# Kernel tuning notes

Hardware: AMD Instinct MI355X
Metric: run time of the kernel (lower is better)

## Reference

```python
import jax, jax.numpy as jnp
import numpy as np

M = 1024      # num_inducing
B = 131072    # batch of query points (original module is per-query; we vmap/vectorize)
EPS_D = 1e-8
JITTER = 1e-4

Z_SCALE = np.array([0.15, 0.1, 0.05, 800.0, 20.0], dtype=np.float32)
Z_SHIFT = np.array([0.0, 0.0, 0.0, 600.0, 5.0], dtype=np.float32)


def setup_inputs() -> dict:
    key = jax.random.key(0)
    k1, k2 = jax.random.split(key)
    x_star = jax.random.normal(k1, (B, 5), dtype=jnp.float32)
    # learnable params, sized/initialized per the flax module
    log_lengthscale = jnp.log(jnp.array([0.2, 0.15, 0.1, 400.0, 15.0], dtype=jnp.float32))
    log_variance = jnp.asarray(jnp.log(0.08), dtype=jnp.float32)
    Z_raw = jax.random.uniform(k2, (M, 5), dtype=jnp.float32)  # uniform(scale=1.0) init
    return {"x_star": x_star, "log_lengthscale": log_lengthscale,
            "log_variance": log_variance, "Z_raw": Z_raw}


def _pairwise_sqdist(A, Bm):
    # ||a-b||^2 via gemm; A:(n,d), Bm:(m,d) -> (n,m)
    aa = jnp.sum(A * A, axis=-1)
    bb = jnp.sum(Bm * Bm, axis=-1)
    d2 = aa[:, None] + bb[None, :] - 2.0 * (A @ Bm.T)
    return jnp.maximum(d2, 0.0)


def _matern52(d2, prior_var):
    d = jnp.sqrt(d2 + EPS_D)
    s = jnp.sqrt(5.0) * d
    return prior_var * (1.0 + s + (5.0 / 3.0) * (d * d)) * jnp.exp(-s)


def reference(x_star, log_lengthscale, log_variance, Z_raw):
    ls = jnp.exp(log_lengthscale)                # (5,)
    prior_var = jnp.exp(log_variance)            # scalar
    Z = Z_raw * jnp.asarray(Z_SCALE) + jnp.asarray(Z_SHIFT)  # (M,5)
    inv_ls = 1.0 / (ls + 1e-8)
    Zs = Z * inv_ls                              # lengthscale-scaled inducing pts
    Xs = x_star * inv_ls                         # (B,5)

    K_ZZ = _matern52(_pairwise_sqdist(Zs, Zs), prior_var)            # (M,M)
    K_ZZ_inv = jnp.linalg.inv(K_ZZ + JITTER * jnp.eye(M, dtype=K_ZZ.dtype))

    k_xZ = _matern52(_pairwise_sqdist(Xs, Zs), prior_var)            # (B,M)
    red = jnp.sum(k_xZ * (k_xZ @ K_ZZ_inv), axis=-1)                 # (B,)
    variance = jnp.maximum(prior_var - red, 1e-6)
    return jnp.sqrt(variance)                                        # (B,) predictive std
```

## Files before the change

### kernel.cpp

```cpp
#include <hip/hip_runtime.h>
#include <math.h>

#define B_TOT 131072
#define M_N   1024
#define BS    128
#define NBK   8

typedef float    f32x4 __attribute__((ext_vector_type(4)));
typedef _Float16 f16x8 __attribute__((ext_vector_type(8)));

enum : size_t {
    OFF_KF  = 0,
    OFF_LF  = (size_t)4 << 20,
    OFF_WF  = (size_t)8 << 20,
    OFF_WPH = (size_t)12 << 20,
    OFF_WPL = (size_t)14 << 20,
    OFF_RED = (size_t)16 << 20,
    OFF_PF  = (size_t)17 << 20,
    OFF_ZT  = ((size_t)17 << 20) + 256,
};

__device__ __constant__ float c_zscale[5] = {0.15f, 0.1f, 0.05f, 800.0f, 20.0f};
__device__ __constant__ float c_zshift[5] = {0.0f, 0.0f, 0.0f, 600.0f, 5.0f};

__global__ __launch_bounds__(256) void k_build(const float* __restrict__ log_ls,
                                               const float* __restrict__ log_var,
                                               const float* __restrict__ Zraw,
                                               float* __restrict__ Kf,
                                               float* __restrict__ pf,
                                               float* __restrict__ Zst) {
    __shared__ float ps[6];
    __shared__ float zsi[5];
    int tid = threadIdx.x;
    if (tid < 5) ps[tid] = 1.0f / (__expf(log_ls[tid]) + 1e-8f);
    if (tid == 5) ps[5] = __expf(log_var[0]);
    __syncthreads();
    int i = blockIdx.x >> 2;
    int j = (blockIdx.x & 3) * 256 + tid;
    if (tid < 5) zsi[tid] = (Zraw[i * 5 + tid] * c_zscale[tid] + c_zshift[tid]) * ps[tid];
    __syncthreads();
    float d2 = 0.0f;
#pragma unroll
    for (int d = 0; d < 5; ++d) {
        float zj = (Zraw[j * 5 + d] * c_zscale[d] + c_zshift[d]) * ps[d];
        float df = zsi[d] - zj;
        d2 += df * df;
    }
    float dd = d2 + 1e-8f;
    float dist = sqrtf(dd);
    float s = 2.23606798f * dist;
    float v = ps[5] * (1.0f + s + 1.66666667f * dd) * __expf(-s);
    if (i == j) v += 1e-4f;
    Kf[(size_t)i * M_N + j] = v;
    if (blockIdx.x < 4) {
        int m = blockIdx.x * 256 + tid;
#pragma unroll
        for (int d = 0; d < 5; ++d)
            Zst[d * M_N + m] = (Zraw[m * 5 + d] * c_zscale[d] + c_zshift[d]) * ps[d];
    }
    if (blockIdx.x == 4 && tid < 6) pf[tid] = ps[tid];
}

__global__ __launch_bounds__(512) void kw_diag(float* __restrict__ Kf,
                                               float* __restrict__ Wf, int kb) {
    __shared__ float As[128][129];
    __shared__ float sinv[128];
    int tid = threadIdx.x;
    int r0 = kb * BS;
    for (int idx = tid; idx < BS * BS; idx += 512) {
        int rr = idx >> 7, cc = idx & 127;
        As[rr][cc] = Kf[(size_t)(r0 + rr) * M_N + r0 + cc];
    }
    __syncthreads();

    int r = tid & 127, q = tid >> 7;
    for (int p = 0; p < 16; ++p) {
        int j0 = p * 8;
        for (int j = j0; j < j0 + 8; ++j) {
            if (tid == j) {
                float d = sqrtf(As[j][j]);
                As[j][j] = d;
                sinv[j] = 1.0f / d;
            }
            __syncthreads();
            float arj = 0.0f;
            if (q == 0 && r > j) {
                arj = As[r][j] * sinv[j];
                As[r][j] = arj;
            }
            __syncthreads();
            if (q == 0 && r > j) {
#pragma unroll
                for (int c = j + 1; c < j0 + 8; ++c)
                    As[r][c] -= arj * As[c][j];
            }
        }
        __syncthreads();
        if (p < 15) {
            float a[8];
#pragma unroll
            for (int t = 0; t < 8; ++t) a[t] = As[r][j0 + t];
            for (int c = j0 + 8 + q; c < 128; c += 4) {
                if (r >= c) {
                    float s = As[r][c];
#pragma unroll
                    for (int t = 0; t < 8; ++t) s -= a[t] * As[c][j0 + t];
                    As[r][c] = s;
                }
            }
        }
        __syncthreads();
    }

    if (tid < 128) {
        int c = tid;
        for (int rb = 0; rb < 16; ++rb) {
            int r0b = rb * 8;
            if (c >= r0b + 8) continue;
            float s[8];
#pragma unroll
            for (int i = 0; i < 8; ++i) s[i] = 0.0f;
            for (int t = 0; t < r0b; ++t) {
                if (t >= c) {
                    float xt = (t == c) ? sinv[c] : As[c][t];
#pragma unroll
                    for (int i = 0; i < 8; ++i) s[i] += As[r0b + i][t] * xt;
                }
            }
            float xloc[8];
#pragma unroll
            for (int i = 0; i < 8; ++i) {
                int rr = r0b + i;
                float v = 0.0f;
                if (rr >= c) {
                    v = ((rr == c) ? 1.0f : 0.0f) - s[i];
#pragma unroll
                    for (int t2 = 0; t2 < i; ++t2) {
                        int tt = r0b + t2;
                        if (tt >= c) v -= As[rr][tt] * xloc[t2];
                    }
                    v *= sinv[rr];
                    if (rr > c) As[c][rr] = v;
                }
                xloc[i] = v;
            }
        }
    }
    __syncthreads();
    for (int idx = tid; idx < BS * BS; idx += 512) {
        int rr = idx >> 7, cc = idx & 127;
        if (rr >= cc)
            Wf[(size_t)(r0 + rr) * M_N + r0 + cc] = (rr == cc) ? sinv[rr] : As[cc][rr];
    }
}

static __device__ void d_strip(const float* __restrict__ Kf, const float* __restrict__ Wf,
                               int cb, int row0, float (*S)[129],
                               float (*Ast)[17], float (*Wst)[128], int tid) {
    int c = tid & 127, q = tid >> 7;
    float acc[32];
#pragma unroll
    for (int i = 0; i < 32; ++i) acc[i] = 0.0f;
    for (int tc = 0; tc < 8; ++tc) {
        int tb = tc * 16;
        __syncthreads();
        for (int idx = tid; idx < 64 * 16; idx += 256) {
            int rr = idx >> 4, tt = idx & 15;
            Ast[rr][tt] = Kf[(size_t)(row0 + rr) * M_N + cb + tb + tt];
        }
        for (int idx = tid; idx < 128 * 16; idx += 256) {
            int cc = idx >> 4, tt = idx & 15;
            Wst[tt][cc] = (tb + tt <= cc) ? Wf[(size_t)(cb + cc) * M_N + cb + tb + tt] : 0.0f;
        }
        __syncthreads();
#pragma unroll
        for (int t = 0; t < 16; ++t) {
            float w = Wst[t][c];
#pragma unroll
            for (int i = 0; i < 32; ++i) acc[i] += Ast[q * 32 + i][t] * w;
        }
    }
#pragma unroll
    for (int i = 0; i < 32; ++i) S[q * 32 + i][c] = acc[i];
}

__global__ __launch_bounds__(256) void kw_step(float* __restrict__ Kf,
                                               const float* __restrict__ Wf,
                                               float* __restrict__ Lf, int kb) {
    __shared__ float SA[64][129];
    __shared__ float SB[64][129];
    __shared__ float Ast[64][17];
    __shared__ float Wst[16][128];
    int tid = threadIdx.x;
    int v = blockIdx.x;
    int by = 0;
    while ((by + 1) * (by + 2) / 2 <= v) ++by;
    int bx = v - by * (by + 1) / 2;
    int base = (kb + 1) * BS;
    int cb = kb * BS;
    int gr0 = base + by * 64, gc0 = base + bx * 64;

    d_strip(Kf, Wf, cb, gr0, SA, Ast, Wst, tid);
    if (bx != by) d_strip(Kf, Wf, cb, gc0, SB, Ast, Wst, tid);
    float (*PB)[129] = (bx == by) ? SA : SB;
    __syncthreads();

    int tx = tid & 15, ty = tid >> 4;
    float acc[4][4];
#pragma unroll
    for (int i = 0; i < 4; ++i)
#pragma unroll
        for (int j = 0; j < 4; ++j) acc[i][j] = 0.0f;
    for (int t = 0; t < 128; ++t) {
        float a[4], b[4];
#pragma unroll
        for (int i = 0; i < 4; ++i) a[i] = SA[ty * 4 + i][t];
#pragma unroll
        for (int j = 0; j < 4; ++j) b[j] = PB[tx * 4 + j][t];
#pragma unroll
        for (int i = 0; i < 4; ++i)
#pragma unroll
            for (int j = 0; j < 4; ++j) acc[i][j] = fmaf(a[i], b[j], acc[i][j]);
    }
#pragma unroll
    for (int i = 0; i < 4; ++i)
#pragma unroll
        for (int j = 0; j < 4; ++j)
            Kf[(size_t)(gr0 + ty * 4 + i) * M_N + gc0 + tx * 4 + j] -= acc[i][j];

    if (by == bx) {
        for (int idx = tid; idx < 64 * 128; idx += 256)
            Lf[(size_t)(gr0 + (idx >> 7)) * M_N + cb + (idx & 127)] = SA[idx >> 7][idx & 127];
    }
}

__global__ __launch_bounds__(512) void kw_trtri(const float* __restrict__ Lf,
                                                float* __restrict__ Wf) {
    __shared__ float Ls[128][33];
    __shared__ float Ws[32][33];
    __shared__ float Whist[6][128][33];
    __shared__ float Ps[128][33];
    int j  = blockIdx.y;
    int ct = blockIdx.x;
    int c0 = j * BS + ct * 32;
    int tid = threadIdx.x;
    int rq = tid >> 2, cq = tid & 3;

    for (int i = j + 1; i < 8; ++i) {
        float acc[8];
#pragma unroll
        for (int c = 0; c < 8; ++c) acc[c] = 0.0f;
        for (int t = j; t < i; ++t) {
            for (int ch = 0; ch < 4; ++ch) {
                int tb = t * BS + ch * 32;
                __syncthreads();
                for (int idx = tid; idx < 128 * 32; idx += 512) {
                    int rr = idx >> 5, tt = idx & 31;
                    Ls[rr][tt] = Lf[(size_t)(i * BS + rr) * M_N + tb + tt];
                }
                if (t == j) {
                    for (int idx = tid; idx < 32 * 32; idx += 512) {
                        int tt = idx >> 5, cc = idx & 31;
                        int gr = tb + tt, gc = c0 + cc;
                        Ws[tt][cc] = (gr >= gc) ? Wf[(size_t)gr * M_N + gc] : 0.0f;
                    }
                }
                __syncthreads();
                if (t == j) {
#pragma unroll
                    for (int tt = 0; tt < 32; ++tt) {
                        float l = Ls[rq][tt];
#pragma unroll
                        for (int c = 0; c < 8; ++c)
                            acc[c] = fmaf(l, Ws[tt][cq * 8 + c], acc[c]);
                    }
                } else {
                    const float (*Wh)[33] = Whist[t - j - 1];
#pragma unroll
                    for (int tt = 0; tt < 32; ++tt) {
                        float l = Ls[rq][tt];
#pragma unroll
                        for (int c = 0; c < 8; ++c)
                            acc[c] = fmaf(l, Wh[ch * 32 + tt][cq * 8 + c], acc[c]);
                    }
                }
            }
        }
        __syncthreads();
#pragma unroll
        for (int c = 0; c < 8; ++c) Ps[rq][cq * 8 + c] = acc[c];
        float a2[8];
#pragma unroll
        for (int c = 0; c < 8; ++c) a2[c] = 0.0f;
        for (int ch = 0; ch < 4; ++ch) {
            __syncthreads();
            for (int idx = tid; idx < 128 * 32; idx += 512) {
                int rr = idx >> 5, tt = idx & 31;
                Ls[rr][tt] = (rr >= ch * 32 + tt)
                           ? Wf[(size_t)(i * BS + rr) * M_N + i * BS + ch * 32 + tt] : 0.0f;
            }
            __syncthreads();
#pragma unroll
            for (int tt = 0; tt < 32; ++tt) {
                float l = Ls[rq][tt];
#pragma unroll
                for (int c = 0; c < 8; ++c)
                    a2[c] = fmaf(l, Ps[ch * 32 + tt][cq * 8 + c], a2[c]);
            }
        }
        __syncthreads();
#pragma unroll
        for (int c = 0; c < 8; ++c) {
            float v = -a2[c];
            Wf[(size_t)(i * BS + rq) * M_N + c0 + cq * 8 + c] = v;
            if (i < 7) Whist[i - j - 1][rq][cq * 8 + c] = v;
        }
        __syncthreads();
    }
}

__global__ void kw_pack(const float* __restrict__ Wf, _Float16* __restrict__ Wph,
                        _Float16* __restrict__ Wpl) {
    int T = blockIdx.x * 256 + threadIdx.x;
    int lane = T & 63, fid = T >> 6;
    int jn = fid & 63, kik = fid >> 6;
    int ki = kik & 3, kc = kik >> 2;
    int j  = jn * 16 + (lane & 15);
    int kb = kc * 128 + ki * 32 + (lane >> 4) * 8;
    f16x8 h, lo;
#pragma unroll
    for (int e = 0; e < 8; ++e) {
        int k = kb + e;
        float v = (k <= j) ? Wf[(size_t)j * M_N + k] : 0.0f;
        _Float16 hh = (_Float16)v;
        h[e]  = hh;
        lo[e] = (_Float16)(v - (float)hh);
    }
    size_t off = (size_t)fid * 512 + lane * 8;
    *(f16x8*)(Wph + off) = h;
    *(f16x8*)(Wpl + off) = lo;
}

__global__ __launch_bounds__(256) void k_mm(const float* __restrict__ x_star,
                                            const float* __restrict__ pf,
                                            const float* __restrict__ Zst,
                                            const _Float16* __restrict__ Wph,
                                            const _Float16* __restrict__ Wpl,
                                            float* __restrict__ redp, int Bq) {
    __shared__ __align__(16) char kls[32 * 256];
    __shared__ float red_l[32];
    int tid  = threadIdx.x;
    int slab = blockIdx.x, pp = blockIdx.y;
    int w = tid >> 6, lane = tid & 63;
    int lrow = lane & 15, kgrp = lane >> 4;

    int srow = tid >> 3, sg = tid & 7;
    int qrow = slab * 32 + srow;
    int qc = (qrow < Bq) ? qrow : (Bq - 1);
    float xv0 = x_star[(size_t)qc * 5 + 0] * pf[0];
    float xv1 = x_star[(size_t)qc * 5 + 1] * pf[1];
    float xv2 = x_star[(size_t)qc * 5 + 2] * pf[2];
    float xv3 = x_star[(size_t)qc * 5 + 3] * pf[3];
    float xv4 = x_star[(size_t)qc * 5 + 4] * pf[4];
    float pv = pf[5];
    if (tid < 32) red_l[tid] = 0.0f;

    f32x4 acc[2][8];
#pragma unroll
    for (int mi = 0; mi < 2; ++mi)
#pragma unroll
        for (int nj = 0; nj < 8; ++nj) acc[mi][nj] = (f32x4)(0.0f);

    int jmax_w = (pp * 32 + 28 + ((w + 3) & 3)) * 16 + 15;
    int KC = pp ? 8 : 4;

    for (int kc = 0; kc < KC; ++kc) {
        f16x8 hv[2];
#pragma unroll
        for (int b = 0; b < 2; ++b) {
            int lb = kc * 128 + sg * 16 + b * 8;
            float z0[8], z1[8], z2[8], z3[8], z4[8];
            *(float4*)&z0[0] = *(const float4*)&Zst[lb];
            *(float4*)&z0[4] = *(const float4*)&Zst[lb + 4];
            *(float4*)&z1[0] = *(const float4*)&Zst[M_N + lb];
            *(float4*)&z1[4] = *(const float4*)&Zst[M_N + lb + 4];
            *(float4*)&z2[0] = *(const float4*)&Zst[2 * M_N + lb];
            *(float4*)&z2[4] = *(const float4*)&Zst[2 * M_N + lb + 4];
            *(float4*)&z3[0] = *(const float4*)&Zst[3 * M_N + lb];
            *(float4*)&z3[4] = *(const float4*)&Zst[3 * M_N + lb + 4];
            *(float4*)&z4[0] = *(const float4*)&Zst[4 * M_N + lb];
            *(float4*)&z4[4] = *(const float4*)&Zst[4 * M_N + lb + 4];
#pragma unroll
            for (int e = 0; e < 8; ++e) {
                float dx0 = xv0 - z0[e], dx1 = xv1 - z1[e], dx2 = xv2 - z2[e],
                      dx3 = xv3 - z3[e], dx4 = xv4 - z4[e];
                float d2 = dx0 * dx0 + dx1 * dx1 + dx2 * dx2 + dx3 * dx3 + dx4 * dx4;
                float ddv = d2 + 1e-8f;
                float dist = sqrtf(ddv);
                float sv = 2.23606798f * dist;
                hv[b][e] = (_Float16)(pv * (1.0f + sv + 1.66666667f * ddv) * __expf(-sv));
            }
        }
        __syncthreads();
        {
            int o0 = srow * 256 + ((sg * 32) ^ ((srow & 15) << 4));
            int o1 = srow * 256 + ((sg * 32 + 16) ^ ((srow & 15) << 4));
            *(f16x8*)(&kls[o0]) = hv[0];
            *(f16x8*)(&kls[o1]) = hv[1];
        }
        __syncthreads();

        for (int ki = 0; ki < 4; ++ki) {
            int kmin = kc * 128 + ki * 32;
            if (kmin > jmax_w) break;
            f16x8 A_[2];
#pragma unroll
            for (int mi = 0; mi < 2; ++mi) {
                int row = mi * 16 + lrow;
                int cb  = ki * 64 + kgrp * 16;
                A_[mi] = *(const f16x8*)(&kls[row * 256 + (cb ^ ((row & 15) << 4))]);
            }
#pragma unroll
            for (int nj = 0; nj < 8; ++nj) {
                int jng = pp * 32 + nj * 4 + ((w + nj) & 3);
                if (kmin > jng * 16 + 15) continue;
                size_t fo = ((size_t)((kc * 4 + ki) * 64 + jng)) * 512 + lane * 8;
                f16x8 Bh = *(const f16x8*)(Wph + fo);
                f16x8 Bl = *(const f16x8*)(Wpl + fo);
#pragma unroll
                for (int mi = 0; mi < 2; ++mi) {
                    acc[mi][nj] = __builtin_amdgcn_mfma_f32_16x16x32_f16(A_[mi], Bh, acc[mi][nj], 0, 0, 0);
                    acc[mi][nj] = __builtin_amdgcn_mfma_f32_16x16x32_f16(A_[mi], Bl, acc[mi][nj], 0, 0, 0);
                }
            }
        }
    }

#pragma unroll
    for (int mi = 0; mi < 2; ++mi) {
#pragma unroll
        for (int q = 0; q < 4; ++q) {
            float s = 0.0f;
#pragma unroll
            for (int nj = 0; nj < 8; ++nj) s = fmaf(acc[mi][nj][q], acc[mi][nj][q], s);
            s += __shfl_xor(s, 1);
            s += __shfl_xor(s, 2);
            s += __shfl_xor(s, 4);
            s += __shfl_xor(s, 8);
            if (lrow == 0) atomicAdd(&red_l[mi * 16 + kgrp * 4 + q], s);
        }
    }
    __syncthreads();
    if (tid < 32) {
        int b = slab * 32 + tid;
        if (b < Bq) redp[(size_t)pp * Bq + b] = red_l[tid];
    }
}

__global__ void k_fin(const float* __restrict__ redp, const float* __restrict__ pf,
                      float* __restrict__ out, int Bq) {
    int b = blockIdx.x * 256 + threadIdx.x;
    if (b < Bq) {
        float red = redp[b] + redp[(size_t)Bq + b];
        out[b] = sqrtf(fmaxf(pf[5] - red, 1e-6f));
    }
}

extern "C" void kernel_launch(void* const* d_in, const int* in_sizes, int n_in,
                              void* d_out, int out_size, void* d_ws, size_t ws_size,
                              hipStream_t stream) {
    const float* x_star  = (const float*)d_in[0];
    const float* log_ls  = (const float*)d_in[1];
    const float* log_var = (const float*)d_in[2];
    const float* Z_raw   = (const float*)d_in[3];
    float* out = (float*)d_out;
    int Bq = in_sizes[0] / 5;

    char* ws = (char*)d_ws;
    float*     Kf   = (float*)(ws + OFF_KF);
    float*     Lf   = (float*)(ws + OFF_LF);
    float*     Wf   = (float*)(ws + OFF_WF);
    _Float16*  Wph  = (_Float16*)(ws + OFF_WPH);
    _Float16*  Wpl  = (_Float16*)(ws + OFF_WPL);
    float*     redp = (float*)(ws + OFF_RED);
    float*     pf   = (float*)(ws + OFF_PF);
    float*     Zst  = (float*)(ws + OFF_ZT);

    k_build<<<4096, 256, 0, stream>>>(log_ls, log_var, Z_raw, Kf, pf, Zst);

    for (int kb = 0; kb < NBK; ++kb) {
        kw_diag<<<1, 512, 0, stream>>>(Kf, Wf, kb);
        int R = M_N - (kb + 1) * BS;
        if (R > 0) {
            int nt = R / 64;
            kw_step<<<nt * (nt + 1) / 2, 256, 0, stream>>>(Kf, Wf, Lf, kb);
        }
    }
    kw_trtri<<<dim3(4, 7), 512, 0, stream>>>(Lf, Wf);
    kw_pack<<<512, 256, 0, stream>>>(Wf, Wph, Wpl);

    int slabs = (Bq + 31) / 32;
    k_mm<<<dim3(slabs, 2), 256, 0, stream>>>(x_star, pf, Zst, Wph, Wpl, redp, Bq);
    k_fin<<<(Bq + 255) / 256, 256, 0, stream>>>(redp, pf, out, Bq);
}
```

Before: 3.555 ms.

## Fuse diagonal factor into step kernel and restructure main MFMA kernel

The blocked Cholesky loop now folds the next diagonal-block factorization and inversion into block 0 of each trailing-update launch, so the separate per-step diag launches go away. The main kernel handles 64 query rows per 512-thread block instead of splitting columns across two blocks with 32 rows each. It also double-buffers the on-the-fly k_xZ tile in LDS so tile generation overlaps the MFMAs, and writes the final sqrt directly, dropping the partial-sum buffer and finalize kernel. The cost is more registers and LDS per block (launch bounds 512,1), lower occupancy, and a serial 256-thread diagonal factorization on the critical path of each step.

Result: slower. 3.680 ms (+3.5%).

```diff
diff --git a/kernel.cpp b/kernel.cpp
--- a/kernel.cpp
+++ b/kernel.cpp
@@ -15,9 +15,8 @@
     OFF_WF  = (size_t)8 << 20,
     OFF_WPH = (size_t)12 << 20,
     OFF_WPL = (size_t)14 << 20,
-    OFF_RED = (size_t)16 << 20,
-    OFF_PF  = (size_t)17 << 20,
-    OFF_ZT  = ((size_t)17 << 20) + 256,
+    OFF_PF  = (size_t)16 << 20,
+    OFF_ZT  = ((size_t)16 << 20) + 256,
 };
 
 __device__ __constant__ float c_zscale[5] = {0.15f, 0.1f, 0.05f, 800.0f, 20.0f};
@@ -180,57 +179,184 @@
             for (int i = 0; i < 32; ++i) acc[i] += Ast[q * 32 + i][t] * w;
         }
     }
+    __syncthreads();
 #pragma unroll
     for (int i = 0; i < 32; ++i) S[q * 32 + i][c] = acc[i];
 }
 
+static __device__ void d_diag256(float (*As)[129], float* sinv,
+                                 float* __restrict__ Wf, int r0, int tid) {
+    int r = tid & 127, half = tid >> 7;
+    for (int p = 0; p < 16; ++p) {
+        int j0 = p * 8;
+        for (int j = j0; j < j0 + 8; ++j) {
+            if (tid == j) {
+                float d = sqrtf(As[j][j]);
+                As[j][j] = d;
+                sinv[j] = 1.0f / d;
+            }
+            __syncthreads();
+            float arj = 0.0f;
+            if (half == 0 && r > j) {
+                arj = As[r][j] * sinv[j];
+                As[r][j] = arj;
+            }
+            __syncthreads();
+            if (half == 0 && r > j) {
+#pragma unroll
+                for (int c = j + 1; c < j0 + 8; ++c)
+                    As[r][c] -= arj * As[c][j];
+            }
+        }
+        __syncthreads();
+        if (p < 15) {
+            float a[8];
+#pragma unroll
+            for (int t = 0; t < 8; ++t) a[t] = As[r][j0 + t];
+            for (int c = j0 + 8 + half; c < 128; c += 2) {
+                if (r >= c) {
+                    float s = As[r][c];
+#pragma unroll
+                    for (int t = 0; t < 8; ++t) s -= a[t] * As[c][j0 + t];
+                    As[r][c] = s;
+                }
+            }
+        }
+        __syncthreads();
+    }
+    if (tid < 128) {
+        int c = tid;
+        for (int rb = 0; rb < 16; ++rb) {
+            int r0b = rb * 8;
+            if (c >= r0b + 8) continue;
+            float s[8];
+#pragma unroll
+            for (int i = 0; i < 8; ++i) s[i] = 0.0f;
+            for (int t = 0; t < r0b; ++t) {
+                if (t >= c) {
+                    float xt = (t == c) ? sinv[c] : As[c][t];
+#pragma unroll
+                    for (int i = 0; i < 8; ++i) s[i] += As[r0b + i][t] * xt;
+                }
+            }
+            float xloc[8];
+#pragma unroll
+            for (int i = 0; i < 8; ++i) {
+                int rr = r0b + i;
+                float v = 0.0f;
+                if (rr >= c) {
+                    v = ((rr == c) ? 1.0f : 0.0f) - s[i];
+#pragma unroll
+                    for (int t2 = 0; t2 < i; ++t2) {
+                        int tt = r0b + t2;
+                        if (tt >= c) v -= As[rr][tt] * xloc[t2];
+                    }
+                    v *= sinv[rr];
+                    if (rr > c) As[c][rr] = v;
+                }
+                xloc[i] = v;
+            }
+        }
+    }
+    __syncthreads();
+    for (int idx = tid; idx < BS * BS; idx += 256) {
+        int rr = idx >> 7, cc = idx & 127;
+        if (rr >= cc)
+            Wf[(size_t)(r0 + rr) * M_N + r0 + cc] = (rr == cc) ? sinv[rr] : As[cc][rr];
+    }
+}
+
 __global__ __launch_bounds__(256) void kw_step(float* __restrict__ Kf,
-                                               const float* __restrict__ Wf,
+                                               float* __restrict__ Wf,
                                                float* __restrict__ Lf, int kb) {
     __shared__ float SA[64][129];
     __shared__ float SB[64][129];
     __shared__ float Ast[64][17];
     __shared__ float Wst[16][128];
+    __shared__ float As[128][129];
+    __shared__ float sinv[128];
     int tid = threadIdx.x;
-    int v = blockIdx.x;
-    int by = 0;
-    while ((by + 1) * (by + 2) / 2 <= v) ++by;
-    int bx = v - by * (by + 1) / 2;
     int base = (kb + 1) * BS;
     int cb = kb * BS;
-    int gr0 = base + by * 64, gc0 = base + bx * 64;
-
-    d_strip(Kf, Wf, cb, gr0, SA, Ast, Wst, tid);
-    if (bx != by) d_strip(Kf, Wf, cb, gc0, SB, Ast, Wst, tid);
-    float (*PB)[129] = (bx == by) ? SA : SB;
-    __syncthreads();
-
     int tx = tid & 15, ty = tid >> 4;
-    float acc[4][4];
-#pragma unroll
-    for (int i = 0; i < 4; ++i)
-#pragma unroll
-        for (int j = 0; j < 4; ++j) acc[i][j] = 0.0f;
-    for (int t = 0; t < 128; ++t) {
-        float a[4], b[4];
-#pragma unroll
-        for (int i = 0; i < 4; ++i) a[i] = SA[ty * 4 + i][t];
-#pragma unroll
-        for (int j = 0; j < 4; ++j) b[j] = PB[tx * 4 + j][t];
+
+    if (blockIdx.x == 0) {
+        d_strip(Kf, Wf, cb, base, SA, Ast, Wst, tid);
+        d_strip(Kf, Wf, cb, base + 64, SB, Ast, Wst, tid);
+        __syncthreads();
+#pragma unroll
+        for (int qq = 0; qq < 3; ++qq) {
+            int qy = (qq == 0) ? 0 : 1;
+            int qx = (qq == 2) ? 1 : 0;
+            float (*Sy)[129] = qy ? SB : SA;
+            float (*Sx)[129] = qx ? SB : SA;
+            float acc[4][4];
+#pragma unroll
+            for (int i = 0; i < 4; ++i)
+#pragma unroll
+                for (int j = 0; j < 4; ++j) acc[i][j] = 0.0f;
+            for (int t = 0; t < 128; ++t) {
+                float a[4], b[4];
+#pragma unroll
+                for (int i = 0; i < 4; ++i) a[i] = Sy[ty * 4 + i][t];
+#pragma unroll
+                for (int j = 0; j < 4; ++j) b[j] = Sx[tx * 4 + j][t];
+#pragma unroll
+                for (int i = 0; i < 4; ++i)
+#pragma unroll
+                    for (int j = 0; j < 4; ++j) acc[i][j] = fmaf(a[i], b[j], acc[i][j]);
+            }
+#pragma unroll
+            for (int i = 0; i < 4; ++i)
+#pragma unroll
+                for (int j = 0; j < 4; ++j)
+                    As[qy * 64 + ty * 4 + i][qx * 64 + tx * 4 + j] =
+                        Kf[(size_t)(base + qy * 64 + ty * 4 + i) * M_N +
+                           base + qx * 64 + tx * 4 + j] - acc[i][j];
+        }
+        for (int idx = tid; idx < 64 * 128; idx += 256) {
+            int rr = idx >> 7, cc = idx & 127;
+            Lf[(size_t)(base + rr) * M_N + cb + cc]      = SA[rr][cc];
+            Lf[(size_t)(base + 64 + rr) * M_N + cb + cc] = SB[rr][cc];
+        }
+        __syncthreads();
+        d_diag256(As, sinv, Wf, base, tid);
+    } else {
+        int vp = blockIdx.x + 2;
+        int by = 0;
+        while ((by + 1) * (by + 2) / 2 <= vp) ++by;
+        int bx = vp - by * (by + 1) / 2;
+        int gr0 = base + by * 64, gc0 = base + bx * 64;
+        d_strip(Kf, Wf, cb, gr0, SA, Ast, Wst, tid);
+        if (bx != by) d_strip(Kf, Wf, cb, gc0, SB, Ast, Wst, tid);
+        float (*PB)[129] = (bx == by) ? SA : SB;
+        __syncthreads();
+        float acc[4][4];
 #pragma unroll
         for (int i = 0; i < 4; ++i)
 #pragma unroll
-            for (int j = 0; j < 4; ++j) acc[i][j] = fmaf(a[i], b[j], acc[i][j]);
-    }
-#pragma unroll
-    for (int i = 0; i < 4; ++i)
-#pragma unroll
-        for (int j = 0; j < 4; ++j)
-            Kf[(size_t)(gr0 + ty * 4 + i) * M_N + gc0 + tx * 4 + j] -= acc[i][j];
-
-    if (by == bx) {
-        for (int idx = tid; idx < 64 * 128; idx += 256)
-            Lf[(size_t)(gr0 + (idx >> 7)) * M_N + cb + (idx & 127)] = SA[idx >> 7][idx & 127];
+            for (int j = 0; j < 4; ++j) acc[i][j] = 0.0f;
+        for (int t = 0; t < 128; ++t) {
+            float a[4], b[4];
+#pragma unroll
+            for (int i = 0; i < 4; ++i) a[i] = SA[ty * 4 + i][t];
+#pragma unroll
+            for (int j = 0; j < 4; ++j) b[j] = PB[tx * 4 + j][t];
+#pragma unroll
+            for (int i = 0; i < 4; ++i)
+#pragma unroll
+                for (int j = 0; j < 4; ++j) acc[i][j] = fmaf(a[i], b[j], acc[i][j]);
+        }
+#pragma unroll
+        for (int i = 0; i < 4; ++i)
+#pragma unroll
+            for (int j = 0; j < 4; ++j)
+                Kf[(size_t)(gr0 + ty * 4 + i) * M_N + gc0 + tx * 4 + j] -= acc[i][j];
+        if (by == bx) {
+            for (int idx = tid; idx < 64 * 128; idx += 256)
+                Lf[(size_t)(gr0 + (idx >> 7)) * M_N + cb + (idx & 127)] =
+                    SA[idx >> 7][idx & 127];
+        }
     }
 }
 
@@ -341,103 +467,116 @@
     *(f16x8*)(Wpl + off) = lo;
 }
 
-__global__ __launch_bounds__(256) void k_mm(const float* __restrict__ x_star,
-                                            const float* __restrict__ pf,
-                                            const float* __restrict__ Zst,
-                                            const _Float16* __restrict__ Wph,
-                                            const _Float16* __restrict__ Wpl,
-                                            float* __restrict__ redp, int Bq) {
-    __shared__ __align__(16) char kls[32 * 256];
-    __shared__ float red_l[32];
+__global__ __launch_bounds__(512, 1) void k_mm(const float* __restrict__ x_star,
+                                               const float* __restrict__ pf,
+                                               const float* __restrict__ Zst,
+                                               const _Float16* __restrict__ Wph,
+                                               const _Float16* __restrict__ Wpl,
+                                               float* __restrict__ out, int Bq) {
+    __shared__ __align__(16) char kls[2][64 * 256];
+    __shared__ float red_l[64];
     int tid  = threadIdx.x;
-    int slab = blockIdx.x, pp = blockIdx.y;
+    int slab = blockIdx.x;
     int w = tid >> 6, lane = tid & 63;
     int lrow = lane & 15, kgrp = lane >> 4;
 
-    int srow = tid >> 3, sg = tid & 7;
-    int qrow = slab * 32 + srow;
-    int qc = (qrow < Bq) ? qrow : (Bq - 1);
-    float xv0 = x_star[(size_t)qc * 5 + 0] * pf[0];
-    float xv1 = x_star[(size_t)qc * 5 + 1] * pf[1];
-    float xv2 = x_star[(size_t)qc * 5 + 2] * pf[2];
-    float xv3 = x_star[(size_t)qc * 5 + 3] * pf[3];
-    float xv4 = x_star[(size_t)qc * 5 + 4] * pf[4];
+    int scc = tid & 15, srow0 = tid >> 4;
+    int q0 = slab * 64 + srow0;
+    int q1 = q0 + 32;
+    int qa = (q0 < Bq) ? q0 : (Bq - 1);
+    int qb = (q1 < Bq) ? q1 : (Bq - 1);
+    float xa0 = x_star[(size_t)qa * 5 + 0] * pf[0];
+    float xa1 = x_star[(size_t)qa * 5 + 1] * pf[1];
+    float xa2 = x_star[(size_t)qa * 5 + 2] * pf[2];
+    float xa3 = x_star[(size_t)qa * 5 + 3] * pf[3];
+    float xa4 = x_star[(size_t)qa * 5 + 4] * pf[4];
+    float xb0 = x_star[(size_t)qb * 5 + 0] * pf[0];
+    float xb1 = x_star[(size_t)qb * 5 + 1] * pf[1];
+    float xb2 = x_star[(size_t)qb * 5 + 2] * pf[2];
+    float xb3 = x_star[(size_t)qb * 5 + 3] * pf[3];
+    float xb4 = x_star[(size_t)qb * 5 + 4] * pf[4];
     float pv = pf[5];
-    if (tid < 32) red_l[tid] = 0.0f;
-
-    f32x4 acc[2][8];
-#pragma unroll
-    for (int mi = 0; mi < 2; ++mi)
+    if (tid < 64) red_l[tid] = 0.0f;
+
+    f32x4 acc[4][8];
+#pragma unroll
+    for (int mi = 0; mi < 4; ++mi)
 #pragma unroll
         for (int nj = 0; nj < 8; ++nj) acc[mi][nj] = (f32x4)(0.0f);
 
-    int jmax_w = (pp * 32 + 28 + ((w + 3) & 3)) * 16 + 15;
-    int KC = pp ? 8 : 4;
-
-    for (int kc = 0; kc < KC; ++kc) {
-        f16x8 hv[2];
-#pragma unroll
-        for (int b = 0; b < 2; ++b) {
-            int lb = kc * 128 + sg * 16 + b * 8;
-            float z0[8], z1[8], z2[8], z3[8], z4[8];
-            *(float4*)&z0[0] = *(const float4*)&Zst[lb];
-            *(float4*)&z0[4] = *(const float4*)&Zst[lb + 4];
-            *(float4*)&z1[0] = *(const float4*)&Zst[M_N + lb];
-            *(float4*)&z1[4] = *(const float4*)&Zst[M_N + lb + 4];
-            *(float4*)&z2[0] = *(const float4*)&Zst[2 * M_N + lb];
-            *(float4*)&z2[4] = *(const float4*)&Zst[2 * M_N + lb + 4];
-            *(float4*)&z3[0] = *(const float4*)&Zst[3 * M_N + lb];
-            *(float4*)&z3[4] = *(const float4*)&Zst[3 * M_N + lb + 4];
-            *(float4*)&z4[0] = *(const float4*)&Zst[4 * M_N + lb];
-            *(float4*)&z4[4] = *(const float4*)&Zst[4 * M_N + lb + 4];
-#pragma unroll
-            for (int e = 0; e < 8; ++e) {
-                float dx0 = xv0 - z0[e], dx1 = xv1 - z1[e], dx2 = xv2 - z2[e],
-                      dx3 = xv3 - z3[e], dx4 = xv4 - z4[e];
+    int jmax_w = (56 + ((w + 7) & 7)) * 16 + 15;
+    int swz = (scc * 16) ^ ((srow0 & 15) << 4);
+    int soff0 = srow0 * 256 + swz;
+    int soff1 = (srow0 + 32) * 256 + swz;
+
+    auto stage = [&](int kc, char* buf) {
+        f16x8 h0, h1;
+#pragma unroll
+        for (int bb = 0; bb < 2; ++bb) {
+            int lb = kc * 128 + scc * 8 + bb * 4;
+            float z0[4], z1[4], z2[4], z3[4], z4[4];
+            *(float4*)z0 = *(const float4*)&Zst[lb];
+            *(float4*)z1 = *(const float4*)&Zst[M_N + lb];
+            *(float4*)z2 = *(const float4*)&Zst[2 * M_N + lb];
+            *(float4*)z3 = *(const float4*)&Zst[3 * M_N + lb];
+            *(float4*)z4 = *(const float4*)&Zst[4 * M_N + lb];
+#pragma unroll
+            for (int e = 0; e < 4; ++e) {
+                float dx0 = xa0 - z0[e], dx1 = xa1 - z1[e], dx2 = xa2 - z2[e],
+                      dx3 = xa3 - z3[e], dx4 = xa4 - z4[e];
                 float d2 = dx0 * dx0 + dx1 * dx1 + dx2 * dx2 + dx3 * dx3 + dx4 * dx4;
                 float ddv = d2 + 1e-8f;
                 float dist = sqrtf(ddv);
                 float sv = 2.23606798f * dist;
-                hv[b][e] = (_Float16)(pv * (1.0f + sv + 1.66666667f * ddv) * __expf(-sv));
-            }
-        }
-        __syncthreads();
-        {
-            int o0 = srow * 256 + ((sg * 32) ^ ((srow & 15) << 4));
-            int o1 = srow * 256 + ((sg * 32 + 16) ^ ((srow & 15) << 4));
-            *(f16x8*)(&kls[o0]) = hv[0];
-            *(f16x8*)(&kls[o1]) = hv[1];
-        }
-        __syncthreads();
-
+                h0[bb * 4 + e] = (_Float16)(pv * (1.0f + sv + 1.66666667f * ddv) * __expf(-sv));
+                float ex0 = xb0 - z0[e], ex1 = xb1 - z1[e], ex2 = xb2 - z2[e],
+                      ex3 = xb3 - z3[e], ex4 = xb4 - z4[e];
+                float e2 = ex0 * ex0 + ex1 * ex1 + ex2 * ex2 + ex3 * ex3 + ex4 * ex4;
+                float eev = e2 + 1e-8f;
+                float edist = sqrtf(eev);
+                float esv = 2.23606798f * edist;
+                h1[bb * 4 + e] = (_Float16)(pv * (1.0f + esv + 1.66666667f * eev) * __expf(-esv));
+            }
+        }
+        *(f16x8*)(&buf[soff0]) = h0;
+        *(f16x8*)(&buf[soff1]) = h1;
+    };
+
+    stage(0, kls[0]);
+    __syncthreads();
+
+    for (int kc = 0; kc < 8; ++kc) {
+        if (kc < 7) stage(kc + 1, kls[(kc + 1) & 1]);
+        const char* cur = kls[kc & 1];
         for (int ki = 0; ki < 4; ++ki) {
             int kmin = kc * 128 + ki * 32;
             if (kmin > jmax_w) break;
-            f16x8 A_[2];
-#pragma unroll
-            for (int mi = 0; mi < 2; ++mi) {
+            f16x8 A_[4];
+#pragma unroll
+            for (int mi = 0; mi < 4; ++mi) {
                 int row = mi * 16 + lrow;
                 int cb  = ki * 64 + kgrp * 16;
-                A_[mi] = *(const f16x8*)(&kls[row * 256 + (cb ^ ((row & 15) << 4))]);
+                A_[mi] = *(const f16x8*)(&cur[row * 256 + (cb ^ ((row & 15) << 4))]);
             }
 #pragma unroll
             for (int nj = 0; nj < 8; ++nj) {
-                int jng = pp * 32 + nj * 4 + ((w + nj) & 3);
+                int jng = nj * 8 + ((w + nj) & 7);
                 if (kmin > jng * 16 + 15) continue;
                 size_t fo = ((size_t)((kc * 4 + ki) * 64 + jng)) * 512 + lane * 8;
                 f16x8 Bh = *(const f16x8*)(Wph + fo);
                 f16x8 Bl = *(const f16x8*)(Wpl + fo);
 #pragma unroll
-                for (int mi = 0; mi < 2; ++mi) {
+                for (int mi = 0; mi < 4; ++mi) {
                     acc[mi][nj] = __builtin_amdgcn_mfma_f32_16x16x32_f16(A_[mi], Bh, acc[mi][nj], 0, 0, 0);
                     acc[mi][nj] = __builtin_amdgcn_mfma_f32_16x16x32_f16(A_[mi], Bl, acc[mi][nj], 0, 0, 0);
                 }
             }
         }
-    }
-
-#pragma unroll
-    for (int mi = 0; mi < 2; ++mi) {
+        __syncthreads();
+    }
+
+#pragma unroll
+    for (int mi = 0; mi < 4; ++mi) {
 #pragma unroll
         for (int q = 0; q < 4; ++q) {
             float s = 0.0f;
@@ -451,18 +590,9 @@
         }
     }
     __syncthreads();
-    if (tid < 32) {
-        int b = slab * 32 + tid;
-        if (b < Bq) redp[(size_t)pp * Bq + b] = red_l[tid];
-    }
-}
-
-__global__ void k_fin(const float* __restrict__ redp, const float* __restrict__ pf,
-                      float* __restrict__ out, int Bq) {
-    int b = blockIdx.x * 256 + threadIdx.x;
-    if (b < Bq) {
-        float red = redp[b] + redp[(size_t)Bq + b];
-        out[b] = sqrtf(fmaxf(pf[5] - red, 1e-6f));
+    if (tid < 64) {
+        int b = slab * 64 + tid;
+        if (b < Bq) out[b] = sqrtf(fmaxf(pv - red_l[tid], 1e-6f));
     }
 }
 
@@ -477,29 +607,26 @@
     int Bq = in_sizes[0] / 5;
 
     char* ws = (char*)d_ws;
-    float*     Kf   = (float*)(ws + OFF_KF);
-    float*     Lf   = (float*)(ws + OFF_LF);
-    float*     Wf   = (float*)(ws + OFF_WF);
-    _Float16*  Wph  = (_Float16*)(ws + OFF_WPH);
-    _Float16*  Wpl  = (_Float16*)(ws + OFF_WPL);
-    float*     redp = (float*)(ws + OFF_RED);
-    float*     pf   = (float*)(ws + OFF_PF);
-    float*     Zst  = (float*)(ws + OFF_ZT);
+    float*     Kf  = (float*)(ws + OFF_KF);
+    float*     Lf  = (float*)(ws + OFF_LF);
+    float*     Wf  = (float*)(ws + OFF_WF);
+    _Float16*  Wph = (_Float16*)(ws + OFF_WPH);
+    _Float16*  Wpl = (_Float16*)(ws + OFF_WPL);
+    float*     pf  = (float*)(ws + OFF_PF);
+    float*     Zst = (float*)(ws + OFF_ZT);
 
     k_build<<<4096, 256, 0, stream>>>(log_ls, log_var, Z_raw, Kf, pf, Zst);
-
-    for (int kb = 0; kb < NBK; ++kb) {
-        kw_diag<<<1, 512, 0, stream>>>(Kf, Wf, kb);
-        int R = M_N - (kb + 1) * BS;
-        if (R > 0) {
-            int nt = R / 64;
-            kw_step<<<nt * (nt + 1) / 2, 256, 0, stream>>>(Kf, Wf, Lf, kb);
-        }
-    }
+    kw_diag<<<1, 512, 0, stream>>>(Kf, Wf, 0);
+
+    for (int kb = 0; kb < NBK - 1; ++kb) {
+        int nt = (NBK - 1 - kb) * 2;
+        int grid = nt * (nt + 1) / 2 - 2;
+        kw_step<<<grid, 256, 0, stream>>>(Kf, Wf, Lf, kb);
+    }
+
     kw_trtri<<<dim3(4, 7), 512, 0, stream>>>(Lf, Wf);
     kw_pack<<<512, 256, 0, stream>>>(Wf, Wph, Wpl);
 
-    int slabs = (Bq + 31) / 32;
-    k_mm<<<dim3(slabs, 2), 256, 0, stream>>>(x_star, pf, Zst, Wph, Wpl, redp, Bq);
-    k_fin<<<(Bq + 255) / 256, 256, 0, stream>>>(redp, pf, out, Bq);
-}
+    int slabs = (Bq + 63) / 64;
+    k_mm<<<slabs, 512, 0, stream>>>(x_star, pf, Zst, Wph, Wpl, out, Bq);
+}
```
